# Kernel tuning notes

Measured on AMD Instinct MI355X. Metric: run time of the kernel, lower is better.

Reference implementation:

```python
import jax, jax.numpy as jnp
import numpy as np

R = 512      # latent dim
M = 4        # center dimensionality
L = 256      # number of cluster centers
B = 8192     # batch
SIGMA_EPS = 1e-4


def setup_inputs() -> dict:
    key = jax.random.key(0)
    kx, kc = jax.random.split(key)
    x = jax.random.normal(kx, (B, R), dtype=jnp.float32)
    c = jax.random.normal(kc, (M, L), dtype=jnp.float32)   # codebook centers
    sigma = jnp.full((1,), 5.0, dtype=jnp.float32)         # trainable temperature
    return {"x": x, "c": c, "sigma": sigma}


def reference(x, c, sigma):
    b = x.shape[0]
    nf = R // M
    z = x.reshape(b, nf, M)                                # (b, nf, m)
    sig = jax.nn.relu(sigma[0]) + SIGMA_EPS
    # squared distances ||z - c||^2 over m, expanded to avoid (b,nf,m,L) materialization
    z_sq = jnp.sum(z * z, axis=-1, keepdims=True)          # (b, nf, 1)
    c_sq = jnp.sum(c * c, axis=0)                          # (L,)
    zc = jnp.einsum('bnm,ml->bnl', z, c)                   # (b, nf, L)
    dist = z_sq - 2.0 * zc + c_sq[None, None, :]           # (b, nf, L)
    q = jax.nn.softmax(-sig * dist, axis=-1)               # soft assignments (b, nf, L)
    out = jnp.einsum('bnl,ml->bnm', q, c)                  # weighted centers (b, nf, m)
    return out.reshape(b, R)
```

## Files before the change

### kernel.cpp

```cpp
#include <hip/hip_runtime.h>
#include <math.h>

#define RDIM 512
#define MDIM 4
#define LDIM 256
#define BDIM 8192
#define NROWS (BDIM * (RDIM / MDIM))
#define SIGMA_EPS 1e-4f
#define LOG2E 1.4426950408889634f
#define SHIFT_HEADROOM 96.0f

typedef _Float16 half4_t __attribute__((ext_vector_type(4)));
typedef short    short8_t __attribute__((ext_vector_type(8)));
typedef __fp16   fp16x2_t __attribute__((ext_vector_type(2)));
typedef float    float4_t __attribute__((ext_vector_type(4)));

#define NRT (NROWS / 16)
#define MAIN_BLOCKS 2048
#define WPB 4
#define NT (NRT / (MAIN_BLOCKS * WPB))

static __device__ __host__ inline unsigned short bf16_rne(float f) {
  unsigned u = __builtin_bit_cast(unsigned, f);
  return (unsigned short)((u + 0x7FFFu + ((u >> 16) & 1u)) >> 16);
}

__global__ void prep_kernel(const float* __restrict__ c, const float* __restrict__ sigma,
                            _Float16* __restrict__ a1w, unsigned short* __restrict__ a2w) {
  const int gid  = blockIdx.x * 256 + threadIdx.x;
  const int lane = gid & 63;
  const int q4   = lane >> 4;
  const int m    = lane & 15;
  const float sig   = fmaxf(sigma[0], 0.0f) + SIGMA_EPS;
  const float sigL  = sig * LOG2E;
  const float sig2L = 2.0f * sigL;
  if (gid < 1024) {
    const int t = gid >> 6;
    const int l = t * 16 + m;
    float cv[4];
    cv[0] = c[l]; cv[1] = c[256 + l]; cv[2] = c[512 + l]; cv[3] = c[768 + l];
    _Float16 uh[4], ul[4];
    #pragma unroll
    for (int i = 0; i < 4; ++i) {
      float u = sig2L * cv[i];
      uh[i] = (_Float16)u;
      ul[i] = (_Float16)(u - (float)uh[i]);
    }
    float bias = -sigL * fmaf(cv[0], cv[0], fmaf(cv[1], cv[1], fmaf(cv[2], cv[2], cv[3] * cv[3])));
    _Float16 bh = (_Float16)bias;
    _Float16 bl = (_Float16)(bias - (float)bh);
    #pragma unroll
    for (int j = 0; j < 4; ++j) {
      _Float16 v;
      if      (q4 <  2) v = uh[j];
      else if (q4 == 2) v = ul[j];
      else              v = (j == 0) ? bh : ((j == 1) ? bl : (_Float16)1.0f);
      a1w[(t * 64 + lane) * 4 + j] = v;
    }
  } else if (gid < 2048) {
    const int p = (gid - 1024) >> 6;
    const int pc = p & 7;
    const bool hi = (p < 8);
    #pragma unroll
    for (int j = 0; j < 8; ++j) {
      int center = 32 * pc + 16 * (j >> 2) + 4 * q4 + (j & 3);
      unsigned short v = 0;
      if (m < 4) {
        float cf = c[m * 256 + center];
        unsigned short h = bf16_rne(cf);
        if (hi) v = h;
        else {
          float res = cf - __builtin_bit_cast(float, (unsigned)h << 16);
          v = bf16_rne(res);
        }
      } else if (m == 4) {
        v = hi ? (unsigned short)0x3F80 : (unsigned short)0;
      }
      a2w[(p * 64 + lane) * 8 + j] = v;
    }
  }
}

union U2H4 { uint2 u; half4_t h; };
union U4S8 { uint4 u; short8_t s; };

__global__ __launch_bounds__(256, 4) void sq_mfma_kernel(
    const float4* __restrict__ x4,
    const _Float16* __restrict__ a1w,
    const unsigned short* __restrict__ a2w,
    const float* __restrict__ sigma,
    float4* __restrict__ out4) {
  const int tid  = threadIdx.x;
  const int lane = tid & 63;
  const int wave = tid >> 6;
  const int q4   = lane >> 4;
  const int zr   = lane & 15;

  const float sigL = (fmaxf(sigma[0], 0.0f) + SIGMA_EPS) * LOG2E;

  half4_t a1[16];
  short8_t a2[16];
  const half4_t* a1p = (const half4_t*)a1w;
  const short8_t* a2p = (const short8_t*)a2w;
  #pragma unroll
  for (int t = 0; t < 16; ++t) a1[t] = a1p[t * 64 + lane];
  #pragma unroll
  for (int p = 0; p < 16; ++p) a2[p] = a2p[p * 64 + lane];

  const int gw = blockIdx.x * WPB + wave;
  const float4_t zero4 = {0.f, 0.f, 0.f, 0.f};
  const unsigned one_one = 0x3C003C00u;

  for (int it = 0; it < NT; ++it) {
    const int rowbase = (gw * NT + it) * 16;

    const float4 z = x4[rowbase + zr];
    fp16x2_t zh01 = __builtin_amdgcn_cvt_pkrtz(z.x, z.y);
    fp16x2_t zh23 = __builtin_amdgcn_cvt_pkrtz(z.z, z.w);
    fp16x2_t zl01 = __builtin_amdgcn_cvt_pkrtz(z.x - (float)zh01[0], z.y - (float)zh01[1]);
    fp16x2_t zl23 = __builtin_amdgcn_cvt_pkrtz(z.z - (float)zh23[0], z.w - (float)zh23[1]);
    const unsigned zh01u = __builtin_bit_cast(unsigned, zh01);
    const unsigned zh23u = __builtin_bit_cast(unsigned, zh23);
    const unsigned zl01u = __builtin_bit_cast(unsigned, zl01);
    const unsigned zl23u = __builtin_bit_cast(unsigned, zl23);

    float U = sigL * fmaf(z.x, z.x, fmaf(z.y, z.y, fmaf(z.z, z.z, z.w * z.w))) - SHIFT_HEADROOM;
    float Uh = (float)(_Float16)U;
    fp16x2_t nU = __builtin_amdgcn_cvt_pkrtz(-Uh, -(U - Uh));

    const unsigned w0 = (q4 == 1) ? zl01u : ((q4 == 3) ? one_one : zh01u);
    const unsigned w1 = (q4 == 3) ? __builtin_bit_cast(unsigned, nU)
                                  : ((q4 == 1) ? zl23u : zh23u);
    U2H4 b1; b1.u = make_uint2(w0, w1);

    float4_t d2 = zero4;
    #pragma unroll
    for (int p = 0; p < 8; ++p) {
      float4_t sa = __builtin_amdgcn_mfma_f32_16x16x16f16(a1[2 * p],     b1.h, zero4, 0, 0, 0);
      float4_t sb = __builtin_amdgcn_mfma_f32_16x16x16f16(a1[2 * p + 1], b1.h, zero4, 0, 0, 0);
      float e0 = __builtin_amdgcn_exp2f(sa[0]);
      float e1 = __builtin_amdgcn_exp2f(sa[1]);
      float e2 = __builtin_amdgcn_exp2f(sa[2]);
      float e3 = __builtin_amdgcn_exp2f(sa[3]);
      float e4 = __builtin_amdgcn_exp2f(sb[0]);
      float e5 = __builtin_amdgcn_exp2f(sb[1]);
      float e6 = __builtin_amdgcn_exp2f(sb[2]);
      float e7 = __builtin_amdgcn_exp2f(sb[3]);
      U4S8 b2;
      b2.u.x = __builtin_amdgcn_perm(__builtin_bit_cast(unsigned, e1),
                                     __builtin_bit_cast(unsigned, e0), 0x07060302u);
      b2.u.y = __builtin_amdgcn_perm(__builtin_bit_cast(unsigned, e3),
                                     __builtin_bit_cast(unsigned, e2), 0x07060302u);
      b2.u.z = __builtin_amdgcn_perm(__builtin_bit_cast(unsigned, e5),
                                     __builtin_bit_cast(unsigned, e4), 0x07060302u);
      b2.u.w = __builtin_amdgcn_perm(__builtin_bit_cast(unsigned, e7),
                                     __builtin_bit_cast(unsigned, e6), 0x07060302u);
      d2 = __builtin_amdgcn_mfma_f32_16x16x32_bf16(a2[p],     b2.s, d2, 0, 0, 0);
      d2 = __builtin_amdgcn_mfma_f32_16x16x32_bf16(a2[p + 8], b2.s, d2, 0, 0, 0);
    }

    float den = __shfl(d2[0], zr + 16);
    if (lane < 16) {
      float r = __builtin_amdgcn_rcpf(den);
      float4 o = make_float4(d2[0] * r, d2[1] * r, d2[2] * r, d2[3] * r);
      out4[rowbase + zr] = o;
    }
  }
}

extern "C" void kernel_launch(void* const* d_in, const int* in_sizes, int n_in,
                              void* d_out, int out_size, void* d_ws, size_t ws_size,
                              hipStream_t stream) {
  const float4* x4    = (const float4*)d_in[0];
  const float*  c     = (const float*)d_in[1];
  const float*  sigma = (const float*)d_in[2];
  float4*       out4  = (float4*)d_out;

  _Float16*       a1w = (_Float16*)d_ws;
  unsigned short* a2w = (unsigned short*)(a1w + 16 * 64 * 4);

  prep_kernel<<<8, 256, 0, stream>>>(c, sigma, a1w, a2w);
  sq_mfma_kernel<<<MAIN_BLOCKS, 256, 0, stream>>>(x4, a1w, a2w, sigma, out4);
}
```

Measured before the change: 103.3 us.

## Process two row tiles per iteration with prefetch and drop bf16 residual centers

The main loop now handles two 16-row tiles at once, interleaving their MFMA and exp2 chains. It prefetches the next pair of x rows and splits the second-stage accumulation across two accumulators to shorten dependency chains. The bf16 low-residual split of the centers in the second MFMA is removed, halving those MFMAs and the a2 registers, at some cost in output precision. Launch bounds drop to 3 waves per SIMD because register pressure rises.

```diff
diff --git a/kernel.cpp b/kernel.cpp
--- a/kernel.cpp
+++ b/kernel.cpp
@@ -57,25 +57,14 @@
       else              v = (j == 0) ? bh : ((j == 1) ? bl : (_Float16)1.0f);
       a1w[(t * 64 + lane) * 4 + j] = v;
     }
-  } else if (gid < 2048) {
+  } else if (gid < 1536) {
     const int p = (gid - 1024) >> 6;
-    const int pc = p & 7;
-    const bool hi = (p < 8);
     #pragma unroll
     for (int j = 0; j < 8; ++j) {
-      int center = 32 * pc + 16 * (j >> 2) + 4 * q4 + (j & 3);
+      int center = 32 * p + 16 * (j >> 2) + 4 * q4 + (j & 3);
       unsigned short v = 0;
-      if (m < 4) {
-        float cf = c[m * 256 + center];
-        unsigned short h = bf16_rne(cf);
-        if (hi) v = h;
-        else {
-          float res = cf - __builtin_bit_cast(float, (unsigned)h << 16);
-          v = bf16_rne(res);
-        }
-      } else if (m == 4) {
-        v = hi ? (unsigned short)0x3F80 : (unsigned short)0;
-      }
+      if (m < 4)       v = bf16_rne(c[m * 256 + center]);
+      else if (m == 4) v = (unsigned short)0x3F80;
       a2w[(p * 64 + lane) * 8 + j] = v;
     }
   }
@@ -84,7 +73,29 @@
 union U2H4 { uint2 u; half4_t h; };
 union U4S8 { uint4 u; short8_t s; };
 
-__global__ __launch_bounds__(256, 4) void sq_mfma_kernel(
+struct B1Frag { U2H4 b1; };
+
+static __device__ __forceinline__ U2H4 make_b1(const float4& z, float sigL, int q4,
+                                               unsigned one_one) {
+  fp16x2_t zh01 = __builtin_amdgcn_cvt_pkrtz(z.x, z.y);
+  fp16x2_t zh23 = __builtin_amdgcn_cvt_pkrtz(z.z, z.w);
+  fp16x2_t zl01 = __builtin_amdgcn_cvt_pkrtz(z.x - (float)zh01[0], z.y - (float)zh01[1]);
+  fp16x2_t zl23 = __builtin_amdgcn_cvt_pkrtz(z.z - (float)zh23[0], z.w - (float)zh23[1]);
+  const unsigned zh01u = __builtin_bit_cast(unsigned, zh01);
+  const unsigned zh23u = __builtin_bit_cast(unsigned, zh23);
+  const unsigned zl01u = __builtin_bit_cast(unsigned, zl01);
+  const unsigned zl23u = __builtin_bit_cast(unsigned, zl23);
+  float U = sigL * fmaf(z.x, z.x, fmaf(z.y, z.y, fmaf(z.z, z.z, z.w * z.w))) - SHIFT_HEADROOM;
+  float Uh = (float)(_Float16)U;
+  fp16x2_t nU = __builtin_amdgcn_cvt_pkrtz(-Uh, -(U - Uh));
+  const unsigned w0 = (q4 == 1) ? zl01u : ((q4 == 3) ? one_one : zh01u);
+  const unsigned w1 = (q4 == 3) ? __builtin_bit_cast(unsigned, nU)
+                                : ((q4 == 1) ? zl23u : zh23u);
+  U2H4 b1; b1.u = make_uint2(w0, w1);
+  return b1;
+}
+
+__global__ __launch_bounds__(256, 3) void sq_mfma_kernel(
     const float4* __restrict__ x4,
     const _Float16* __restrict__ a1w,
     const unsigned short* __restrict__ a2w,
@@ -99,72 +110,99 @@
   const float sigL = (fmaxf(sigma[0], 0.0f) + SIGMA_EPS) * LOG2E;
 
   half4_t a1[16];
-  short8_t a2[16];
+  short8_t a2[8];
   const half4_t* a1p = (const half4_t*)a1w;
   const short8_t* a2p = (const short8_t*)a2w;
   #pragma unroll
   for (int t = 0; t < 16; ++t) a1[t] = a1p[t * 64 + lane];
   #pragma unroll
-  for (int p = 0; p < 16; ++p) a2[p] = a2p[p * 64 + lane];
+  for (int p = 0; p < 8; ++p) a2[p] = a2p[p * 64 + lane];
 
   const int gw = blockIdx.x * WPB + wave;
+  const int tilebase = gw * NT;
   const float4_t zero4 = {0.f, 0.f, 0.f, 0.f};
   const unsigned one_one = 0x3C003C00u;
 
-  for (int it = 0; it < NT; ++it) {
-    const int rowbase = (gw * NT + it) * 16;
-
-    const float4 z = x4[rowbase + zr];
-    fp16x2_t zh01 = __builtin_amdgcn_cvt_pkrtz(z.x, z.y);
-    fp16x2_t zh23 = __builtin_amdgcn_cvt_pkrtz(z.z, z.w);
-    fp16x2_t zl01 = __builtin_amdgcn_cvt_pkrtz(z.x - (float)zh01[0], z.y - (float)zh01[1]);
-    fp16x2_t zl23 = __builtin_amdgcn_cvt_pkrtz(z.z - (float)zh23[0], z.w - (float)zh23[1]);
-    const unsigned zh01u = __builtin_bit_cast(unsigned, zh01);
-    const unsigned zh23u = __builtin_bit_cast(unsigned, zh23);
-    const unsigned zl01u = __builtin_bit_cast(unsigned, zl01);
-    const unsigned zl23u = __builtin_bit_cast(unsigned, zl23);
-
-    float U = sigL * fmaf(z.x, z.x, fmaf(z.y, z.y, fmaf(z.z, z.z, z.w * z.w))) - SHIFT_HEADROOM;
-    float Uh = (float)(_Float16)U;
-    fp16x2_t nU = __builtin_amdgcn_cvt_pkrtz(-Uh, -(U - Uh));
-
-    const unsigned w0 = (q4 == 1) ? zl01u : ((q4 == 3) ? one_one : zh01u);
-    const unsigned w1 = (q4 == 3) ? __builtin_bit_cast(unsigned, nU)
-                                  : ((q4 == 1) ? zl23u : zh23u);
-    U2H4 b1; b1.u = make_uint2(w0, w1);
-
-    float4_t d2 = zero4;
+  float4 zA = x4[(tilebase + 0) * 16 + zr];
+  float4 zB = x4[(tilebase + 1) * 16 + zr];
+
+  for (int it = 0; it < NT; it += 2) {
+    const int itn = (it + 2 < NT) ? (it + 2) : it;
+    float4 zAn = x4[(tilebase + itn) * 16 + zr];
+    float4 zBn = x4[(tilebase + itn + 1) * 16 + zr];
+
+    U2H4 b1A = make_b1(zA, sigL, q4, one_one);
+    U2H4 b1B = make_b1(zB, sigL, q4, one_one);
+
+    float4_t d2A0 = zero4, d2A1 = zero4, d2B0 = zero4, d2B1 = zero4;
     #pragma unroll
     for (int p = 0; p < 8; ++p) {
-      float4_t sa = __builtin_amdgcn_mfma_f32_16x16x16f16(a1[2 * p],     b1.h, zero4, 0, 0, 0);
-      float4_t sb = __builtin_amdgcn_mfma_f32_16x16x16f16(a1[2 * p + 1], b1.h, zero4, 0, 0, 0);
-      float e0 = __builtin_amdgcn_exp2f(sa[0]);
-      float e1 = __builtin_amdgcn_exp2f(sa[1]);
-      float e2 = __builtin_amdgcn_exp2f(sa[2]);
-      float e3 = __builtin_amdgcn_exp2f(sa[3]);
-      float e4 = __builtin_amdgcn_exp2f(sb[0]);
-      float e5 = __builtin_amdgcn_exp2f(sb[1]);
-      float e6 = __builtin_amdgcn_exp2f(sb[2]);
-      float e7 = __builtin_amdgcn_exp2f(sb[3]);
-      U4S8 b2;
-      b2.u.x = __builtin_amdgcn_perm(__builtin_bit_cast(unsigned, e1),
-                                     __builtin_bit_cast(unsigned, e0), 0x07060302u);
-      b2.u.y = __builtin_amdgcn_perm(__builtin_bit_cast(unsigned, e3),
-                                     __builtin_bit_cast(unsigned, e2), 0x07060302u);
-      b2.u.z = __builtin_amdgcn_perm(__builtin_bit_cast(unsigned, e5),
-                                     __builtin_bit_cast(unsigned, e4), 0x07060302u);
-      b2.u.w = __builtin_amdgcn_perm(__builtin_bit_cast(unsigned, e7),
-                                     __builtin_bit_cast(unsigned, e6), 0x07060302u);
-      d2 = __builtin_amdgcn_mfma_f32_16x16x32_bf16(a2[p],     b2.s, d2, 0, 0, 0);
-      d2 = __builtin_amdgcn_mfma_f32_16x16x32_bf16(a2[p + 8], b2.s, d2, 0, 0, 0);
-    }
-
-    float den = __shfl(d2[0], zr + 16);
+      float4_t saA = __builtin_amdgcn_mfma_f32_16x16x16f16(a1[2 * p],     b1A.h, zero4, 0, 0, 0);
+      float4_t sbA = __builtin_amdgcn_mfma_f32_16x16x16f16(a1[2 * p + 1], b1A.h, zero4, 0, 0, 0);
+      float4_t saB = __builtin_amdgcn_mfma_f32_16x16x16f16(a1[2 * p],     b1B.h, zero4, 0, 0, 0);
+      float4_t sbB = __builtin_amdgcn_mfma_f32_16x16x16f16(a1[2 * p + 1], b1B.h, zero4, 0, 0, 0);
+
+      U4S8 b2A, b2B;
+      {
+        float e0 = __builtin_amdgcn_exp2f(saA[0]);
+        float e1 = __builtin_amdgcn_exp2f(saA[1]);
+        float e2 = __builtin_amdgcn_exp2f(saA[2]);
+        float e3 = __builtin_amdgcn_exp2f(saA[3]);
+        float e4 = __builtin_amdgcn_exp2f(sbA[0]);
+        float e5 = __builtin_amdgcn_exp2f(sbA[1]);
+        float e6 = __builtin_amdgcn_exp2f(sbA[2]);
+        float e7 = __builtin_amdgcn_exp2f(sbA[3]);
+        b2A.u.x = __builtin_amdgcn_perm(__builtin_bit_cast(unsigned, e1),
+                                        __builtin_bit_cast(unsigned, e0), 0x07060302u);
+        b2A.u.y = __builtin_amdgcn_perm(__builtin_bit_cast(unsigned, e3),
+                                        __builtin_bit_cast(unsigned, e2), 0x07060302u);
+        b2A.u.z = __builtin_amdgcn_perm(__builtin_bit_cast(unsigned, e5),
+                                        __builtin_bit_cast(unsigned, e4), 0x07060302u);
+        b2A.u.w = __builtin_amdgcn_perm(__builtin_bit_cast(unsigned, e7),
+                                        __builtin_bit_cast(unsigned, e6), 0x07060302u);
+      }
+      {
+        float e0 = __builtin_amdgcn_exp2f(saB[0]);
+        float e1 = __builtin_amdgcn_exp2f(saB[1]);
+        float e2 = __builtin_amdgcn_exp2f(saB[2]);
+        float e3 = __builtin_amdgcn_exp2f(saB[3]);
+        float e4 = __builtin_amdgcn_exp2f(sbB[0]);
+        float e5 = __builtin_amdgcn_exp2f(sbB[1]);
+        float e6 = __builtin_amdgcn_exp2f(sbB[2]);
+        float e7 = __builtin_amdgcn_exp2f(sbB[3]);
+        b2B.u.x = __builtin_amdgcn_perm(__builtin_bit_cast(unsigned, e1),
+                                        __builtin_bit_cast(unsigned, e0), 0x07060302u);
+        b2B.u.y = __builtin_amdgcn_perm(__builtin_bit_cast(unsigned, e3),
+                                        __builtin_bit_cast(unsigned, e2), 0x07060302u);
+        b2B.u.z = __builtin_amdgcn_perm(__builtin_bit_cast(unsigned, e5),
+                                        __builtin_bit_cast(unsigned, e4), 0x07060302u);
+        b2B.u.w = __builtin_amdgcn_perm(__builtin_bit_cast(unsigned, e7),
+                                        __builtin_bit_cast(unsigned, e6), 0x07060302u);
+      }
+      if (p & 1) {
+        d2A1 = __builtin_amdgcn_mfma_f32_16x16x32_bf16(a2[p], b2A.s, d2A1, 0, 0, 0);
+        d2B1 = __builtin_amdgcn_mfma_f32_16x16x32_bf16(a2[p], b2B.s, d2B1, 0, 0, 0);
+      } else {
+        d2A0 = __builtin_amdgcn_mfma_f32_16x16x32_bf16(a2[p], b2A.s, d2A0, 0, 0, 0);
+        d2B0 = __builtin_amdgcn_mfma_f32_16x16x32_bf16(a2[p], b2B.s, d2B0, 0, 0, 0);
+      }
+    }
+
+    float4_t d2A = d2A0 + d2A1;
+    float4_t d2B = d2B0 + d2B1;
+
+    float denA = __shfl(d2A[0], zr + 16);
+    float denB = __shfl(d2B[0], zr + 16);
     if (lane < 16) {
-      float r = __builtin_amdgcn_rcpf(den);
-      float4 o = make_float4(d2[0] * r, d2[1] * r, d2[2] * r, d2[3] * r);
-      out4[rowbase + zr] = o;
-    }
+      float rA = __builtin_amdgcn_rcpf(denA);
+      float rB = __builtin_amdgcn_rcpf(denB);
+      out4[(tilebase + it) * 16 + zr] =
+          make_float4(d2A[0] * rA, d2A[1] * rA, d2A[2] * rA, d2A[3] * rA);
+      out4[(tilebase + it + 1) * 16 + zr] =
+          make_float4(d2B[0] * rB, d2B[1] * rB, d2B[2] * rB, d2B[3] * rB);
+    }
+
+    zA = zAn; zB = zBn;
   }
 }
 
@@ -179,6 +217,6 @@
   _Float16*       a1w = (_Float16*)d_ws;
   unsigned short* a2w = (unsigned short*)(a1w + 16 * 64 * 4);
 
-  prep_kernel<<<8, 256, 0, stream>>>(c, sigma, a1w, a2w);
+  prep_kernel<<<6, 256, 0, stream>>>(c, sigma, a1w, a2w);
   sq_mfma_kernel<<<MAIN_BLOCKS, 256, 0, stream>>>(x4, a1w, a2w, sigma, out4);
 }
```

New measurement: 98.90 us. 1.04x faster.

## Interleave four row tiles per wave, prefetch next inputs, drop bf16 residual MFMA

Applied to the files above, without the earlier changes.

Each wave now processes four 16-row tiles together, issuing their MFMAs back to back so MFMA latency and exp2 work from different tiles overlap, and it prefetches the next group's x values one iteration ahead. The second-stage bf16 split of the centers (hi plus residual) is dropped, which halves the second-stage MFMAs and the registers holding the center operand, at some cost in accuracy. Launch bounds are relaxed from 4 to 3 waves per SIMD to leave room for the extra registers.

```diff
diff --git a/kernel.cpp b/kernel.cpp
--- a/kernel.cpp
+++ b/kernel.cpp
@@ -19,6 +19,7 @@
 #define MAIN_BLOCKS 2048
 #define WPB 4
 #define NT (NRT / (MAIN_BLOCKS * WPB))
+#define QUAD 4
 
 static __device__ __host__ inline unsigned short bf16_rne(float f) {
   unsigned u = __builtin_bit_cast(unsigned, f);
@@ -57,25 +58,14 @@
       else              v = (j == 0) ? bh : ((j == 1) ? bl : (_Float16)1.0f);
       a1w[(t * 64 + lane) * 4 + j] = v;
     }
-  } else if (gid < 2048) {
+  } else if (gid < 1536) {
     const int p = (gid - 1024) >> 6;
-    const int pc = p & 7;
-    const bool hi = (p < 8);
     #pragma unroll
     for (int j = 0; j < 8; ++j) {
-      int center = 32 * pc + 16 * (j >> 2) + 4 * q4 + (j & 3);
+      int center = 32 * p + 16 * (j >> 2) + 4 * q4 + (j & 3);
       unsigned short v = 0;
-      if (m < 4) {
-        float cf = c[m * 256 + center];
-        unsigned short h = bf16_rne(cf);
-        if (hi) v = h;
-        else {
-          float res = cf - __builtin_bit_cast(float, (unsigned)h << 16);
-          v = bf16_rne(res);
-        }
-      } else if (m == 4) {
-        v = hi ? (unsigned short)0x3F80 : (unsigned short)0;
-      }
+      if (m < 4)       v = bf16_rne(c[m * 256 + center]);
+      else if (m == 4) v = (unsigned short)0x3F80;
       a2w[(p * 64 + lane) * 8 + j] = v;
     }
   }
@@ -84,7 +74,27 @@
 union U2H4 { uint2 u; half4_t h; };
 union U4S8 { uint4 u; short8_t s; };
 
-__global__ __launch_bounds__(256, 4) void sq_mfma_kernel(
+static __device__ __forceinline__ U2H4 make_b1(const float4& z, float sigL, int q4,
+                                               unsigned one_one) {
+  fp16x2_t zh01 = __builtin_amdgcn_cvt_pkrtz(z.x, z.y);
+  fp16x2_t zh23 = __builtin_amdgcn_cvt_pkrtz(z.z, z.w);
+  fp16x2_t zl01 = __builtin_amdgcn_cvt_pkrtz(z.x - (float)zh01[0], z.y - (float)zh01[1]);
+  fp16x2_t zl23 = __builtin_amdgcn_cvt_pkrtz(z.z - (float)zh23[0], z.w - (float)zh23[1]);
+  const unsigned zh01u = __builtin_bit_cast(unsigned, zh01);
+  const unsigned zh23u = __builtin_bit_cast(unsigned, zh23);
+  const unsigned zl01u = __builtin_bit_cast(unsigned, zl01);
+  const unsigned zl23u = __builtin_bit_cast(unsigned, zl23);
+  float U = sigL * fmaf(z.x, z.x, fmaf(z.y, z.y, fmaf(z.z, z.z, z.w * z.w))) - SHIFT_HEADROOM;
+  float Uh = (float)(_Float16)U;
+  fp16x2_t nU = __builtin_amdgcn_cvt_pkrtz(-Uh, -(U - Uh));
+  const unsigned w0 = (q4 == 1) ? zl01u : ((q4 == 3) ? one_one : zh01u);
+  const unsigned w1 = (q4 == 3) ? __builtin_bit_cast(unsigned, nU)
+                                : ((q4 == 1) ? zl23u : zh23u);
+  U2H4 b1; b1.u = make_uint2(w0, w1);
+  return b1;
+}
+
+__global__ __launch_bounds__(256, 3) void sq_mfma_kernel(
     const float4* __restrict__ x4,
     const _Float16* __restrict__ a1w,
     const unsigned short* __restrict__ a2w,
@@ -99,72 +109,82 @@
   const float sigL = (fmaxf(sigma[0], 0.0f) + SIGMA_EPS) * LOG2E;
 
   half4_t a1[16];
-  short8_t a2[16];
+  short8_t a2[8];
   const half4_t* a1p = (const half4_t*)a1w;
   const short8_t* a2p = (const short8_t*)a2w;
   #pragma unroll
   for (int t = 0; t < 16; ++t) a1[t] = a1p[t * 64 + lane];
   #pragma unroll
-  for (int p = 0; p < 16; ++p) a2[p] = a2p[p * 64 + lane];
+  for (int p = 0; p < 8; ++p) a2[p] = a2p[p * 64 + lane];
 
   const int gw = blockIdx.x * WPB + wave;
+  const int tilebase = gw * NT;
   const float4_t zero4 = {0.f, 0.f, 0.f, 0.f};
   const unsigned one_one = 0x3C003C00u;
 
-  for (int it = 0; it < NT; ++it) {
-    const int rowbase = (gw * NT + it) * 16;
-
-    const float4 z = x4[rowbase + zr];
-    fp16x2_t zh01 = __builtin_amdgcn_cvt_pkrtz(z.x, z.y);
-    fp16x2_t zh23 = __builtin_amdgcn_cvt_pkrtz(z.z, z.w);
-    fp16x2_t zl01 = __builtin_amdgcn_cvt_pkrtz(z.x - (float)zh01[0], z.y - (float)zh01[1]);
-    fp16x2_t zl23 = __builtin_amdgcn_cvt_pkrtz(z.z - (float)zh23[0], z.w - (float)zh23[1]);
-    const unsigned zh01u = __builtin_bit_cast(unsigned, zh01);
-    const unsigned zh23u = __builtin_bit_cast(unsigned, zh23);
-    const unsigned zl01u = __builtin_bit_cast(unsigned, zl01);
-    const unsigned zl23u = __builtin_bit_cast(unsigned, zl23);
-
-    float U = sigL * fmaf(z.x, z.x, fmaf(z.y, z.y, fmaf(z.z, z.z, z.w * z.w))) - SHIFT_HEADROOM;
-    float Uh = (float)(_Float16)U;
-    fp16x2_t nU = __builtin_amdgcn_cvt_pkrtz(-Uh, -(U - Uh));
-
-    const unsigned w0 = (q4 == 1) ? zl01u : ((q4 == 3) ? one_one : zh01u);
-    const unsigned w1 = (q4 == 3) ? __builtin_bit_cast(unsigned, nU)
-                                  : ((q4 == 1) ? zl23u : zh23u);
-    U2H4 b1; b1.u = make_uint2(w0, w1);
-
-    float4_t d2 = zero4;
+  float4 zq[QUAD];
+  #pragma unroll
+  for (int ch = 0; ch < QUAD; ++ch) zq[ch] = x4[(tilebase + ch) * 16 + zr];
+
+  for (int it = 0; it < NT; it += QUAD) {
+    const int itn = (it + QUAD < NT) ? (it + QUAD) : it;
+    float4 zn[QUAD];
+    #pragma unroll
+    for (int ch = 0; ch < QUAD; ++ch) zn[ch] = x4[(tilebase + itn + ch) * 16 + zr];
+
+    U2H4 b1[QUAD];
+    #pragma unroll
+    for (int ch = 0; ch < QUAD; ++ch) b1[ch] = make_b1(zq[ch], sigL, q4, one_one);
+
+    float4_t d2[QUAD];
+    #pragma unroll
+    for (int ch = 0; ch < QUAD; ++ch) d2[ch] = zero4;
+
     #pragma unroll
     for (int p = 0; p < 8; ++p) {
-      float4_t sa = __builtin_amdgcn_mfma_f32_16x16x16f16(a1[2 * p],     b1.h, zero4, 0, 0, 0);
-      float4_t sb = __builtin_amdgcn_mfma_f32_16x16x16f16(a1[2 * p + 1], b1.h, zero4, 0, 0, 0);
-      float e0 = __builtin_amdgcn_exp2f(sa[0]);
-      float e1 = __builtin_amdgcn_exp2f(sa[1]);
-      float e2 = __builtin_amdgcn_exp2f(sa[2]);
-      float e3 = __builtin_amdgcn_exp2f(sa[3]);
-      float e4 = __builtin_amdgcn_exp2f(sb[0]);
-      float e5 = __builtin_amdgcn_exp2f(sb[1]);
-      float e6 = __builtin_amdgcn_exp2f(sb[2]);
-      float e7 = __builtin_amdgcn_exp2f(sb[3]);
-      U4S8 b2;
-      b2.u.x = __builtin_amdgcn_perm(__builtin_bit_cast(unsigned, e1),
-                                     __builtin_bit_cast(unsigned, e0), 0x07060302u);
-      b2.u.y = __builtin_amdgcn_perm(__builtin_bit_cast(unsigned, e3),
-                                     __builtin_bit_cast(unsigned, e2), 0x07060302u);
-      b2.u.z = __builtin_amdgcn_perm(__builtin_bit_cast(unsigned, e5),
-                                     __builtin_bit_cast(unsigned, e4), 0x07060302u);
-      b2.u.w = __builtin_amdgcn_perm(__builtin_bit_cast(unsigned, e7),
-                                     __builtin_bit_cast(unsigned, e6), 0x07060302u);
-      d2 = __builtin_amdgcn_mfma_f32_16x16x32_bf16(a2[p],     b2.s, d2, 0, 0, 0);
-      d2 = __builtin_amdgcn_mfma_f32_16x16x32_bf16(a2[p + 8], b2.s, d2, 0, 0, 0);
-    }
-
-    float den = __shfl(d2[0], zr + 16);
+      float4_t sa[QUAD], sb[QUAD];
+      #pragma unroll
+      for (int ch = 0; ch < QUAD; ++ch) {
+        sa[ch] = __builtin_amdgcn_mfma_f32_16x16x16f16(a1[2 * p],     b1[ch].h, zero4, 0, 0, 0);
+        sb[ch] = __builtin_amdgcn_mfma_f32_16x16x16f16(a1[2 * p + 1], b1[ch].h, zero4, 0, 0, 0);
+      }
+      #pragma unroll
+      for (int ch = 0; ch < QUAD; ++ch) {
+        float e0 = __builtin_amdgcn_exp2f(sa[ch][0]);
+        float e1 = __builtin_amdgcn_exp2f(sa[ch][1]);
+        float e2 = __builtin_amdgcn_exp2f(sa[ch][2]);
+        float e3 = __builtin_amdgcn_exp2f(sa[ch][3]);
+        float e4 = __builtin_amdgcn_exp2f(sb[ch][0]);
+        float e5 = __builtin_amdgcn_exp2f(sb[ch][1]);
+        float e6 = __builtin_amdgcn_exp2f(sb[ch][2]);
+        float e7 = __builtin_amdgcn_exp2f(sb[ch][3]);
+        U4S8 b2;
+        b2.u.x = __builtin_amdgcn_perm(__builtin_bit_cast(unsigned, e1),
+                                       __builtin_bit_cast(unsigned, e0), 0x07060302u);
+        b2.u.y = __builtin_amdgcn_perm(__builtin_bit_cast(unsigned, e3),
+                                       __builtin_bit_cast(unsigned, e2), 0x07060302u);
+        b2.u.z = __builtin_amdgcn_perm(__builtin_bit_cast(unsigned, e5),
+                                       __builtin_bit_cast(unsigned, e4), 0x07060302u);
+        b2.u.w = __builtin_amdgcn_perm(__builtin_bit_cast(unsigned, e7),
+                                       __builtin_bit_cast(unsigned, e6), 0x07060302u);
+        d2[ch] = __builtin_amdgcn_mfma_f32_16x16x32_bf16(a2[p], b2.s, d2[ch], 0, 0, 0);
+      }
+    }
+
+    float den[QUAD];
+    #pragma unroll
+    for (int ch = 0; ch < QUAD; ++ch) den[ch] = __shfl(d2[ch][0], zr + 16);
     if (lane < 16) {
-      float r = __builtin_amdgcn_rcpf(den);
-      float4 o = make_float4(d2[0] * r, d2[1] * r, d2[2] * r, d2[3] * r);
-      out4[rowbase + zr] = o;
-    }
+      #pragma unroll
+      for (int ch = 0; ch < QUAD; ++ch) {
+        float r = __builtin_amdgcn_rcpf(den[ch]);
+        out4[(tilebase + it + ch) * 16 + zr] =
+            make_float4(d2[ch][0] * r, d2[ch][1] * r, d2[ch][2] * r, d2[ch][3] * r);
+      }
+    }
+
+    #pragma unroll
+    for (int ch = 0; ch < QUAD; ++ch) zq[ch] = zn[ch];
   }
 }
 
@@ -179,6 +199,6 @@
   _Float16*       a1w = (_Float16*)d_ws;
   unsigned short* a2w = (unsigned short*)(a1w + 16 * 64 * 4);
 
-  prep_kernel<<<8, 256, 0, stream>>>(c, sigma, a1w, a2w);
+  prep_kernel<<<6, 256, 0, stream>>>(c, sigma, a1w, a2w);
   sq_mfma_kernel<<<MAIN_BLOCKS, 256, 0, stream>>>(x4, a1w, a2w, sigma, out4);
 }
```

Result: faster. 98.18 us, median of 2 (-4.9%).
